# Performance work log

Hardware: AMD Instinct MI355X
Metric: run time of the kernel (lower is better)

The kernel has to match this reference:

```python
import jax, jax.numpy as jnp
import numpy as np

GAMMA = 1.0  # init arg gamma


def setup_inputs() -> dict:
    key = jax.random.key(0)
    k1, k2 = jax.random.split(key, 2)
    B, D, U = 8192, 512, 4096
    x = jax.random.normal(k1, (B, D), dtype=jnp.float32)
    kernel = jax.random.normal(k2, (D, U), dtype=jnp.float32) * 0.05  # glorot-ish scale
    bias = jnp.zeros((U,), dtype=jnp.float32)
    return {"x": x, "kernel": kernel, "bias": bias}


def reference(x, kernel, bias):
    # Original: distance = ||x[b,:] - kernel[:,u]||_2 over input_dim, out = exp(-gamma*distance^2) + bias.
    # Use the algebraic cdist expansion ||a-b||^2 = |a|^2 + |b|^2 - 2 a.b to avoid
    # materializing the (B, D, U) broadcast tensor the TF code creates.
    x_sq = jnp.sum(x * x, axis=-1, keepdims=True)          # (B, 1)
    k_sq = jnp.sum(kernel * kernel, axis=0)[None, :]       # (1, U)
    d2 = x_sq + k_sq - 2.0 * (x @ kernel)                  # (B, U) squared distances
    d2 = jnp.maximum(d2, 0.0)                              # guard tiny negatives from cancellation
    return jnp.exp(-GAMMA * d2) + bias                     # activation is None (linear)
```

## Files before the change

kernel.cpp:

```cpp
#include <hip/hip_runtime.h>
#include <hip/hip_bf16.h>
#include <stdint.h>


using short8 = __attribute__((ext_vector_type(8))) short;
using bf16x8 = __attribute__((ext_vector_type(8))) __bf16;
using f32x4  = __attribute__((ext_vector_type(4))) float;

#define GAMMA_F 1.0f

__device__ __forceinline__ unsigned short f2bf(float f) {
  unsigned u = __float_as_uint(f);
  u = (u + 0x7fffu + ((u >> 16) & 1u)) >> 16;
  return (unsigned short)u;
}

__global__ __launch_bounds__(256) void prep_x_kernel(const float* __restrict__ x,
                                                     unsigned short* __restrict__ xb,
                                                     float* __restrict__ xsq) {
  const int w = threadIdx.x >> 6, l = threadIdx.x & 63;
  const int r = blockIdx.x * 4 + w;
  const float4* xr = (const float4*)(x + (size_t)r * 512);
  float4 v0 = xr[l * 2 + 0];
  float4 v1 = xr[l * 2 + 1];
  float s = v0.x * v0.x + v0.y * v0.y + v0.z * v0.z + v0.w * v0.w
          + v1.x * v1.x + v1.y * v1.y + v1.z * v1.z + v1.w * v1.w;
  short8 p;
  p[0] = (short)f2bf(v0.x); p[1] = (short)f2bf(v0.y);
  p[2] = (short)f2bf(v0.z); p[3] = (short)f2bf(v0.w);
  p[4] = (short)f2bf(v1.x); p[5] = (short)f2bf(v1.y);
  p[6] = (short)f2bf(v1.z); p[7] = (short)f2bf(v1.w);
  *(short8*)(xb + (size_t)r * 512 + l * 8) = p;
#pragma unroll
  for (int o = 32; o > 0; o >>= 1) s += __shfl_xor(s, o);
  if (l == 0) xsq[r] = s;
}

__global__ __launch_bounds__(256) void prep_kT_kernel(const float* __restrict__ kern,
                                                      unsigned short* __restrict__ kbT,
                                                      float* __restrict__ ksq) {
  __shared__ unsigned short tile[64][65];
  const int t = threadIdx.x;
  const int u0 = blockIdx.x * 64, d0 = blockIdx.y * 64;
  const int c = t & 63, tq = t >> 6;
  float part = 0.f;
#pragma unroll
  for (int i = 0; i < 16; ++i) {
    const int r = tq * 16 + i;
    const float v = kern[(size_t)(d0 + r) * 4096 + u0 + c];
    part += v * v;
    tile[r][c] = f2bf(v);
  }
  atomicAdd(&ksq[u0 + c], part);
  __syncthreads();
  const int dl = (t & 7) * 8;
#pragma unroll
  for (int h = 0; h < 2; ++h) {
    const int ul = (t >> 3) + h * 32;
    short8 v;
#pragma unroll
    for (int j = 0; j < 8; ++j) ((unsigned short*)&v)[j] = tile[dl + j][ul];
    *(short8*)(kbT + (size_t)(u0 + ul) * 512 + d0 + dl) = v;
  }
}

__global__ __launch_bounds__(256) void rbf_gemm_kernel(
    const unsigned short* __restrict__ xb, const unsigned short* __restrict__ kbT,
    const float* __restrict__ xsq, const float* __restrict__ ksq,
    const float* __restrict__ bias, float* __restrict__ out) {
  __shared__ unsigned short As[128 * 64];
  __shared__ unsigned short Bs[128 * 64];
  const int tid = threadIdx.x;
  const int w = tid >> 6, l = tid & 63;
  const int brow = blockIdx.y * 128, bcol = blockIdx.x * 128;
  const int wr = w >> 1, wc = w & 1;

  f32x4 acc[4][4] = {};

  const int srow = tid >> 3;
  const int scol = (tid & 7) * 8;
  const unsigned short* ga = xb + (size_t)(brow + srow) * 512 + scol;
  const unsigned short* gb = kbT + (size_t)(bcol + srow) * 512 + scol;
  unsigned short* lA = &As[w * 512];
  unsigned short* lB = &Bs[w * 512];

  for (int kk = 0; kk < 8; ++kk) {
    const int go = kk * 64;
#pragma unroll
    for (int i = 0; i < 4; ++i)
      __builtin_amdgcn_global_load_lds(
          (const __attribute__((address_space(1))) void*)(ga + (size_t)i * 32 * 512 + go),
          (__attribute__((address_space(3))) void*)(lA + i * 2048), 16, 0, 0);
#pragma unroll
    for (int i = 0; i < 4; ++i)
      __builtin_amdgcn_global_load_lds(
          (const __attribute__((address_space(1))) void*)(gb + (size_t)i * 32 * 512 + go),
          (__attribute__((address_space(3))) void*)(lB + i * 2048), 16, 0, 0);
    __syncthreads();
#pragma unroll
    for (int ki = 0; ki < 2; ++ki) {
      const int ko = ki * 32 + (l >> 4) * 8;
      bf16x8 a[4], b[4];
#pragma unroll
      for (int m = 0; m < 4; ++m)
        a[m] = *(const bf16x8*)&As[(wr * 64 + m * 16 + (l & 15)) * 64 + ko];
#pragma unroll
      for (int n = 0; n < 4; ++n)
        b[n] = *(const bf16x8*)&Bs[(wc * 64 + n * 16 + (l & 15)) * 64 + ko];
#pragma unroll
      for (int m = 0; m < 4; ++m)
#pragma unroll
        for (int n = 0; n < 4; ++n)
          acc[m][n] = __builtin_amdgcn_mfma_f32_16x16x32_bf16(a[m], b[n], acc[m][n], 0, 0, 0);
    }
    __syncthreads();
  }

  const int cl = l & 15, rg = (l >> 4) * 4;
#pragma unroll
  for (int n = 0; n < 4; ++n) {
    const int gc = bcol + wc * 64 + n * 16 + cl;
    const float kq = ksq[gc];
    const float bz = bias[gc];
#pragma unroll
    for (int m = 0; m < 4; ++m) {
      const int gr = brow + wr * 64 + m * 16 + rg;
      const float4 xq = *(const float4*)&xsq[gr];
      const float xq4[4] = {xq.x, xq.y, xq.z, xq.w};
#pragma unroll
      for (int j = 0; j < 4; ++j) {
        float d2 = xq4[j] + kq - 2.0f * acc[m][n][j];
        d2 = fmaxf(d2, 0.0f);
        out[(size_t)(gr + j) * 4096 + gc] = __expf(-GAMMA_F * d2) + bz;
      }
    }
  }
}

__global__ __launch_bounds__(256) void rbf_direct_kernel(
    const float* __restrict__ x, const float* __restrict__ kern,
    const float* __restrict__ bias, float* __restrict__ out) {
  __shared__ float Xs[64][17];
  __shared__ float Ks[16][65];
  const int tid = threadIdx.x;
  const int brow = blockIdx.y * 64, bcol = blockIdx.x * 64;
  const int tr = (tid >> 4) * 4, tc = (tid & 15) * 4;
  float acc[4][4] = {};
  for (int k0 = 0; k0 < 512; k0 += 16) {
    {
      const int r = tid >> 2, c = (tid & 3) * 4;
      float4 v = *(const float4*)&x[(size_t)(brow + r) * 512 + k0 + c];
      Xs[r][c] = v.x; Xs[r][c + 1] = v.y; Xs[r][c + 2] = v.z; Xs[r][c + 3] = v.w;
    }
    {
      const int r = tid >> 4, c = (tid & 15) * 4;
      float4 v = *(const float4*)&kern[(size_t)(k0 + r) * 4096 + bcol + c];
      Ks[r][c] = v.x; Ks[r][c + 1] = v.y; Ks[r][c + 2] = v.z; Ks[r][c + 3] = v.w;
    }
    __syncthreads();
#pragma unroll
    for (int kk = 0; kk < 16; ++kk) {
      float a[4], b[4];
#pragma unroll
      for (int i = 0; i < 4; ++i) a[i] = Xs[tr + i][kk];
#pragma unroll
      for (int j = 0; j < 4; ++j) b[j] = Ks[kk][tc + j];
#pragma unroll
      for (int i = 0; i < 4; ++i)
#pragma unroll
        for (int j = 0; j < 4; ++j) {
          float d = a[i] - b[j];
          acc[i][j] = fmaf(d, d, acc[i][j]);
        }
    }
    __syncthreads();
  }
#pragma unroll
  for (int i = 0; i < 4; ++i)
#pragma unroll
    for (int j = 0; j < 4; ++j)
      out[(size_t)(brow + tr + i) * 4096 + bcol + tc + j] =
          __expf(-GAMMA_F * acc[i][j]) + bias[bcol + tc + j];
}

extern "C" void kernel_launch(void* const* d_in, const int* in_sizes, int n_in,
                              void* d_out, int out_size, void* d_ws, size_t ws_size,
                              hipStream_t stream) {
  const float* x    = (const float*)d_in[0];
  const float* kern = (const float*)d_in[1];
  const float* bias = (const float*)d_in[2];
  float* out = (float*)d_out;

  const size_t NEED = 8388608  + 4194304  + 32768  + 16384 ;
  if (ws_size < NEED) {
    rbf_direct_kernel<<<dim3(64, 128), 256, 0, stream>>>(x, kern, bias, out);
    return;
  }

  char* ws = (char*)d_ws;
  unsigned short* xb  = (unsigned short*)(ws);
  unsigned short* kbT = (unsigned short*)(ws + 8388608);
  float* xsq = (float*)(ws + 8388608 + 4194304);
  float* ksq = xsq + 8192;

  hipMemsetAsync(ksq, 0, 4096 * sizeof(float), stream);
  prep_x_kernel<<<2048, 256, 0, stream>>>(x, xb, xsq);
  prep_kT_kernel<<<dim3(64, 8), 256, 0, stream>>>(kern, kbT, ksq);
  rbf_gemm_kernel<<<dim3(32, 64), 256, 0, stream>>>(xb, kbT, xsq, ksq, bias, out);
}
```

Before: 200.5 us.

## Fuse prep kernels and rewrite GEMM with 256x256 double-buffered swizzled tiles

Merges the x-prep, kernel-transpose prep and memset into one launch, replacing the atomic ksq accumulation with a per-block loop and a shared-memory reduction. The GEMM becomes a 512-thread, 256x256-tile kernel with double-buffered LDS staging, an XOR-swizzled LDS layout to avoid bank conflicts, raised wave priority around MFMA bursts, and a remapped block order for L2 locality. The aim is to cut launch overhead and hide global-load latency behind MFMA work. The cost is much more LDS per block (128 KB) and more accumulator registers, which limits occupancy.

Measured after the change: 214.7 us. 1.07x slower.

```diff
diff --git a/kernel.cpp b/kernel.cpp
--- a/kernel.cpp
+++ b/kernel.cpp
@@ -6,135 +6,178 @@
 using short8 = __attribute__((ext_vector_type(8))) short;
 using bf16x8 = __attribute__((ext_vector_type(8))) __bf16;
 using f32x4  = __attribute__((ext_vector_type(4))) float;
+typedef unsigned short ushort_t;
 
 #define GAMMA_F 1.0f
 
-__device__ __forceinline__ unsigned short f2bf(float f) {
+__device__ __forceinline__ ushort_t f2bf(float f) {
   unsigned u = __float_as_uint(f);
   u = (u + 0x7fffu + ((u >> 16) & 1u)) >> 16;
-  return (unsigned short)u;
-}
-
-__global__ __launch_bounds__(256) void prep_x_kernel(const float* __restrict__ x,
-                                                     unsigned short* __restrict__ xb,
-                                                     float* __restrict__ xsq) {
-  const int w = threadIdx.x >> 6, l = threadIdx.x & 63;
-  const int r = blockIdx.x * 4 + w;
-  const float4* xr = (const float4*)(x + (size_t)r * 512);
-  float4 v0 = xr[l * 2 + 0];
-  float4 v1 = xr[l * 2 + 1];
-  float s = v0.x * v0.x + v0.y * v0.y + v0.z * v0.z + v0.w * v0.w
-          + v1.x * v1.x + v1.y * v1.y + v1.z * v1.z + v1.w * v1.w;
-  short8 p;
-  p[0] = (short)f2bf(v0.x); p[1] = (short)f2bf(v0.y);
-  p[2] = (short)f2bf(v0.z); p[3] = (short)f2bf(v0.w);
-  p[4] = (short)f2bf(v1.x); p[5] = (short)f2bf(v1.y);
-  p[6] = (short)f2bf(v1.z); p[7] = (short)f2bf(v1.w);
-  *(short8*)(xb + (size_t)r * 512 + l * 8) = p;
-#pragma unroll
-  for (int o = 32; o > 0; o >>= 1) s += __shfl_xor(s, o);
-  if (l == 0) xsq[r] = s;
-}
-
-__global__ __launch_bounds__(256) void prep_kT_kernel(const float* __restrict__ kern,
-                                                      unsigned short* __restrict__ kbT,
-                                                      float* __restrict__ ksq) {
-  __shared__ unsigned short tile[64][65];
+  return (ushort_t)u;
+}
+
+__global__ __launch_bounds__(256) void prep_kernel(
+    const float* __restrict__ x, const float* __restrict__ kern,
+    ushort_t* __restrict__ xb, ushort_t* __restrict__ kbT,
+    float* __restrict__ xsq, float* __restrict__ ksq) {
   const int t = threadIdx.x;
-  const int u0 = blockIdx.x * 64, d0 = blockIdx.y * 64;
-  const int c = t & 63, tq = t >> 6;
-  float part = 0.f;
-#pragma unroll
-  for (int i = 0; i < 16; ++i) {
-    const int r = tq * 16 + i;
-    const float v = kern[(size_t)(d0 + r) * 4096 + u0 + c];
-    part += v * v;
-    tile[r][c] = f2bf(v);
-  }
-  atomicAdd(&ksq[u0 + c], part);
-  __syncthreads();
-  const int dl = (t & 7) * 8;
-#pragma unroll
-  for (int h = 0; h < 2; ++h) {
-    const int ul = (t >> 3) + h * 32;
-    short8 v;
-#pragma unroll
-    for (int j = 0; j < 8; ++j) ((unsigned short*)&v)[j] = tile[dl + j][ul];
-    *(short8*)(kbT + (size_t)(u0 + ul) * 512 + d0 + dl) = v;
-  }
-}
-
-__global__ __launch_bounds__(256) void rbf_gemm_kernel(
-    const unsigned short* __restrict__ xb, const unsigned short* __restrict__ kbT,
+  if (blockIdx.x < 2048) {
+    const int w = t >> 6, l = t & 63;
+    const int r = blockIdx.x * 4 + w;
+    const float4* xr = (const float4*)(x + (size_t)r * 512);
+    float4 v0 = xr[l * 2 + 0];
+    float4 v1 = xr[l * 2 + 1];
+    float s = v0.x * v0.x + v0.y * v0.y + v0.z * v0.z + v0.w * v0.w
+            + v1.x * v1.x + v1.y * v1.y + v1.z * v1.z + v1.w * v1.w;
+    short8 p;
+    p[0] = (short)f2bf(v0.x); p[1] = (short)f2bf(v0.y);
+    p[2] = (short)f2bf(v0.z); p[3] = (short)f2bf(v0.w);
+    p[4] = (short)f2bf(v1.x); p[5] = (short)f2bf(v1.y);
+    p[6] = (short)f2bf(v1.z); p[7] = (short)f2bf(v1.w);
+    *(short8*)(xb + (size_t)r * 512 + l * 8) = p;
+#pragma unroll
+    for (int o = 32; o > 0; o >>= 1) s += __shfl_xor(s, o);
+    if (l == 0) xsq[r] = s;
+  } else {
+    __shared__ ushort_t tile[64][65];
+    __shared__ float red[4][64];
+    const int u0 = (blockIdx.x - 2048) * 64;
+    const int c = t & 63, tq = t >> 6;
+    float part = 0.f;
+    for (int d0 = 0; d0 < 512; d0 += 64) {
+#pragma unroll
+      for (int i = 0; i < 16; ++i) {
+        const int r = tq * 16 + i;
+        const float v = kern[(size_t)(d0 + r) * 4096 + u0 + c];
+        part += v * v;
+        tile[r][c] = f2bf(v);
+      }
+      __syncthreads();
+      const int dl = (t & 7) * 8;
+#pragma unroll
+      for (int h = 0; h < 2; ++h) {
+        const int ul = (t >> 3) + h * 32;
+        short8 v;
+#pragma unroll
+        for (int j = 0; j < 8; ++j) ((ushort_t*)&v)[j] = tile[dl + j][ul];
+        *(short8*)(kbT + (size_t)(u0 + ul) * 512 + d0 + dl) = v;
+      }
+      __syncthreads();
+    }
+    red[tq][c] = part;
+    __syncthreads();
+    if (t < 64) ksq[u0 + t] = red[0][t] + red[1][t] + red[2][t] + red[3][t];
+  }
+}
+
+__global__ __launch_bounds__(512, 2) void rbf_gemm8_kernel(
+    const ushort_t* __restrict__ xb, const ushort_t* __restrict__ kbT,
     const float* __restrict__ xsq, const float* __restrict__ ksq,
     const float* __restrict__ bias, float* __restrict__ out) {
-  __shared__ unsigned short As[128 * 64];
-  __shared__ unsigned short Bs[128 * 64];
+  __shared__ ushort_t A_lds[2 * 256 * 64];
+  __shared__ ushort_t B_lds[2 * 256 * 64];
+
   const int tid = threadIdx.x;
   const int w = tid >> 6, l = tid & 63;
-  const int brow = blockIdx.y * 128, bcol = blockIdx.x * 128;
-  const int wr = w >> 1, wc = w & 1;
-
-  f32x4 acc[4][4] = {};
+  const int wr = w >> 2, wc = w & 3;
+
+  const int tile = ((blockIdx.x & 7) << 6) + (blockIdx.x >> 3);
+  const int brow = (tile >> 4) * 256;
+  const int bcol = (tile & 15) * 256;
 
   const int srow = tid >> 3;
-  const int scol = (tid & 7) * 8;
-  const unsigned short* ga = xb + (size_t)(brow + srow) * 512 + scol;
-  const unsigned short* gb = kbT + (size_t)(bcol + srow) * 512 + scol;
-  unsigned short* lA = &As[w * 512];
-  unsigned short* lB = &Bs[w * 512];
-
-  for (int kk = 0; kk < 8; ++kk) {
-    const int go = kk * 64;
-#pragma unroll
-    for (int i = 0; i < 4; ++i)
-      __builtin_amdgcn_global_load_lds(
-          (const __attribute__((address_space(1))) void*)(ga + (size_t)i * 32 * 512 + go),
-          (__attribute__((address_space(3))) void*)(lA + i * 2048), 16, 0, 0);
-#pragma unroll
-    for (int i = 0; i < 4; ++i)
-      __builtin_amdgcn_global_load_lds(
-          (const __attribute__((address_space(1))) void*)(gb + (size_t)i * 32 * 512 + go),
-          (__attribute__((address_space(3))) void*)(lB + i * 2048), 16, 0, 0);
-    __syncthreads();
-#pragma unroll
-    for (int ki = 0; ki < 2; ++ki) {
-      const int ko = ki * 32 + (l >> 4) * 8;
-      bf16x8 a[4], b[4];
-#pragma unroll
-      for (int m = 0; m < 4; ++m)
-        a[m] = *(const bf16x8*)&As[(wr * 64 + m * 16 + (l & 15)) * 64 + ko];
-#pragma unroll
-      for (int n = 0; n < 4; ++n)
-        b[n] = *(const bf16x8*)&Bs[(wc * 64 + n * 16 + (l & 15)) * 64 + ko];
-#pragma unroll
-      for (int m = 0; m < 4; ++m)
-#pragma unroll
-        for (int n = 0; n < 4; ++n)
-          acc[m][n] = __builtin_amdgcn_mfma_f32_16x16x32_bf16(a[m], b[n], acc[m][n], 0, 0, 0);
-    }
-    __syncthreads();
-  }
-
-  const int cl = l & 15, rg = (l >> 4) * 4;
+  const int sj = (tid & 7) ^ ((tid >> 3) & 7);
+  const ushort_t* gA0 = xb  + (size_t)(brow + srow) * 512 + sj * 8;
+  const ushort_t* gB0 = kbT + (size_t)(bcol + srow) * 512 + sj * 8;
+  const int ldsw = w * 512;
+
+#define STAGE_TILE(kt, dn) do {                                                   \
+    const ushort_t* _ga = gA0 + (size_t)(kt) * 64;                                \
+    const ushort_t* _gb = gB0 + (size_t)(kt) * 64;                                \
+    const int _lb = (dn) * 16384 + ldsw;                                          \
+    _Pragma("unroll")                                                             \
+    for (int i = 0; i < 4; ++i)                                                   \
+      __builtin_amdgcn_global_load_lds(                                           \
+          (const __attribute__((address_space(1))) void*)(_ga + (size_t)i * 32768),\
+          (__attribute__((address_space(3))) void*)(&A_lds[_lb + i * 4096]), 16, 0, 0); \
+    _Pragma("unroll")                                                             \
+    for (int i = 0; i < 4; ++i)                                                   \
+      __builtin_amdgcn_global_load_lds(                                           \
+          (const __attribute__((address_space(1))) void*)(_gb + (size_t)i * 32768),\
+          (__attribute__((address_space(3))) void*)(&B_lds[_lb + i * 4096]), 16, 0, 0); \
+  } while (0)
+
+  const int l15 = l & 15, l4 = l >> 4, l7 = l & 7;
+  const int chk0 = (l4 ^ l7) * 8;
+  const int chk1 = ((4 + l4) ^ l7) * 8;
+  const int aoff = (wr * 128 + l15) * 64;
+  const int boff = (wc * 64 + l15) * 64;
+
+  f32x4 acc[8][4] = {};
+
+#define MFMA_PHASE(mh, nh, dbase) do {                                            \
+    bf16x8 _a[4][2], _b[2][2];                                                    \
+    _Pragma("unroll")                                                             \
+    for (int i = 0; i < 4; ++i) {                                                 \
+      _a[i][0] = *(const bf16x8*)&A_lds[(dbase) + aoff + ((mh)*4 + i) * 1024 + chk0]; \
+      _a[i][1] = *(const bf16x8*)&A_lds[(dbase) + aoff + ((mh)*4 + i) * 1024 + chk1]; \
+    }                                                                             \
+    _Pragma("unroll")                                                             \
+    for (int j = 0; j < 2; ++j) {                                                 \
+      _b[j][0] = *(const bf16x8*)&B_lds[(dbase) + boff + ((nh)*2 + j) * 1024 + chk0]; \
+      _b[j][1] = *(const bf16x8*)&B_lds[(dbase) + boff + ((nh)*2 + j) * 1024 + chk1]; \
+    }                                                                             \
+    asm volatile("s_barrier" ::: "memory");                                       \
+    __builtin_amdgcn_s_setprio(1);                                                \
+    _Pragma("unroll")                                                             \
+    for (int i = 0; i < 4; ++i)                                                   \
+      _Pragma("unroll")                                                           \
+      for (int j = 0; j < 2; ++j) {                                               \
+        acc[(mh)*4 + i][(nh)*2 + j] = __builtin_amdgcn_mfma_f32_16x16x32_bf16(    \
+            _a[i][0], _b[j][0], acc[(mh)*4 + i][(nh)*2 + j], 0, 0, 0);            \
+        acc[(mh)*4 + i][(nh)*2 + j] = __builtin_amdgcn_mfma_f32_16x16x32_bf16(    \
+            _a[i][1], _b[j][1], acc[(mh)*4 + i][(nh)*2 + j], 0, 0, 0);            \
+      }                                                                           \
+    __builtin_amdgcn_s_setprio(0);                                                \
+    __builtin_amdgcn_sched_barrier(0);                                            \
+    asm volatile("s_barrier" ::: "memory");                                       \
+  } while (0)
+
+  STAGE_TILE(0, 0);
+
+#pragma unroll 2
+  for (int s = 0; s < 8; ++s) {
+    const int dbase = (s & 1) * 16384;
+    STAGE_TILE((s + 1) & 7, (s + 1) & 1);
+    asm volatile("s_waitcnt vmcnt(8)" ::: "memory");
+    asm volatile("s_barrier" ::: "memory");
+    MFMA_PHASE(0, 0, dbase);
+    MFMA_PHASE(0, 1, dbase);
+    MFMA_PHASE(1, 0, dbase);
+    MFMA_PHASE(1, 1, dbase);
+  }
+
+  const int cl = l15, rg = l4 * 4;
 #pragma unroll
   for (int n = 0; n < 4; ++n) {
     const int gc = bcol + wc * 64 + n * 16 + cl;
     const float kq = ksq[gc];
     const float bz = bias[gc];
 #pragma unroll
-    for (int m = 0; m < 4; ++m) {
-      const int gr = brow + wr * 64 + m * 16 + rg;
-      const float4 xq = *(const float4*)&xsq[gr];
+    for (int m = 0; m < 8; ++m) {
+      const int gr0 = brow + wr * 128 + m * 16 + rg;
+      const float4 xq = *(const float4*)&xsq[gr0];
       const float xq4[4] = {xq.x, xq.y, xq.z, xq.w};
 #pragma unroll
       for (int j = 0; j < 4; ++j) {
         float d2 = xq4[j] + kq - 2.0f * acc[m][n][j];
         d2 = fmaxf(d2, 0.0f);
-        out[(size_t)(gr + j) * 4096 + gc] = __expf(-GAMMA_F * d2) + bz;
+        out[(size_t)(gr0 + j) * 4096 + gc] = __expf(-GAMMA_F * d2) + bz;
       }
     }
   }
+#undef STAGE_TILE
+#undef MFMA_PHASE
 }
 
 __global__ __launch_bounds__(256) void rbf_direct_kernel(
@@ -198,13 +241,11 @@
   }
 
   char* ws = (char*)d_ws;
-  unsigned short* xb  = (unsigned short*)(ws);
-  unsigned short* kbT = (unsigned short*)(ws + 8388608);
+  ushort_t* xb  = (ushort_t*)(ws);
+  ushort_t* kbT = (ushort_t*)(ws + 8388608);
   float* xsq = (float*)(ws + 8388608 + 4194304);
   float* ksq = xsq + 8192;
 
-  hipMemsetAsync(ksq, 0, 4096 * sizeof(float), stream);
-  prep_x_kernel<<<2048, 256, 0, stream>>>(x, xb, xsq);
-  prep_kT_kernel<<<dim3(64, 8), 256, 0, stream>>>(kern, kbT, ksq);
-  rbf_gemm_kernel<<<dim3(32, 64), 256, 0, stream>>>(xb, kbT, xsq, ksq, bias, out);
-}
+  prep_kernel<<<2112, 256, 0, stream>>>(x, kern, xb, kbT, xsq, ksq);
+  rbf_gemm8_kernel<<<512, 512, 0, stream>>>(xb, kbT, xsq, ksq, bias, out);
+}
```
